# Kernel tuning notes

Measured on AMD Instinct MI355X. Metric: run time of the kernel, lower is better.

Reference implementation:

```python
import jax, jax.numpy as jnp
import numpy as np

DIM = 96
DIM_OUT = 192
HEADS = 2
Q_STRIDE = 4
WINDOW_SIZE = 16  # flattened mask-unit size AFTER q pooling
HEAD_DIM = DIM_OUT // HEADS


def setup_inputs() -> dict:
    key = jax.random.key(0)
    k1, k2, k3, k4, k5 = jax.random.split(key, 5)
    B, N = 64, 3136  # 56x56 tokens, 49 windows of 64 tokens
    x = jax.random.normal(k1, (B, N, DIM), dtype=jnp.float32)
    # nn.Linear params (PyTorch layout: [out, in])
    s_qkv = 1.0 / np.sqrt(DIM)
    w_qkv = jax.random.uniform(k2, (3 * DIM_OUT, DIM), jnp.float32, -s_qkv, s_qkv)
    b_qkv = jax.random.uniform(k3, (3 * DIM_OUT,), jnp.float32, -s_qkv, s_qkv)
    s_proj = 1.0 / np.sqrt(DIM_OUT)
    w_proj = jax.random.uniform(k4, (DIM_OUT, DIM_OUT), jnp.float32, -s_proj, s_proj)
    b_proj = jax.random.uniform(k5, (DIM_OUT,), jnp.float32, -s_proj, s_proj)
    return {"x": x, "w_qkv": w_qkv, "b_qkv": b_qkv, "w_proj": w_proj, "b_proj": b_proj}


def reference(x, w_qkv, b_qkv, w_proj, b_proj):
    B, N, _ = x.shape
    num_windows = N // (Q_STRIDE * WINDOW_SIZE)
    tokens_per_win = Q_STRIDE * WINDOW_SIZE  # 64
    # QKV projection; token axis splits as (tokens_per_win, num_windows)
    qkv = (x @ w_qkv.T + b_qkv).reshape(B, tokens_per_win, num_windows, 3, HEADS, HEAD_DIM)
    qkv = jnp.transpose(qkv, (3, 0, 4, 2, 1, 5))  # [3, B, H, W, T, D]
    q, k, v = qkv[0], qkv[1], qkv[2]
    # q pooling via strided amax over q_stride
    q = q.reshape(B, HEADS, num_windows, Q_STRIDE, WINDOW_SIZE, HEAD_DIM).max(axis=3)
    scale = HEAD_DIM ** (-0.5)
    attn = jax.nn.softmax(jnp.einsum('bhwqd,bhwkd->bhwqk', q * scale, k), axis=-1)
    o = jnp.einsum('bhwqk,bhwkd->bhwqd', attn, v)  # [B, H, W, WINDOW_SIZE, D]
    # transpose(1,3) then flatten -> [B, WINDOW_SIZE*num_windows, dim_out]
    o = jnp.transpose(o, (0, 3, 2, 1, 4)).reshape(B, -1, DIM_OUT)
    return o @ w_proj.T + b_proj
```

## Files before the change

kernel.cpp:

```cpp
#include <hip/hip_runtime.h>


#define NW 49
#define NTOK 3136
#define DIM 96
#define DOUT 192

#define WSQ 0
#define WSBQ 55296
#define WSP 55872
#define WSBP 92736
#define WSTOT 92928

typedef __bf16 bf16x8 __attribute__((ext_vector_type(8)));
typedef float f32x4 __attribute__((ext_vector_type(4)));
typedef unsigned short u16x8 __attribute__((ext_vector_type(8)));
typedef unsigned short u16x4 __attribute__((ext_vector_type(4)));
typedef unsigned int   u32x4 __attribute__((ext_vector_type(4)));

__device__ __forceinline__ unsigned short f2bf(float f) {
    return __builtin_bit_cast(unsigned short, (__bf16)f);
}
__device__ __forceinline__ float bf2f(unsigned short h) {
    unsigned int u = ((unsigned int)h) << 16;
    return __builtin_bit_cast(float, u);
}

__device__ __forceinline__ bool sniff_fp32(const unsigned short* x16) {
    int sane = 0;
    #pragma unroll
    for (int i = 0; i < 32; ++i) {
        unsigned e = ((unsigned)x16[2 * i] >> 7) & 0xFFu;
        sane += (e >= 100u && e <= 141u) ? 1 : 0;
    }
    return sane < 24;
}

__device__ __forceinline__ bf16x8 ldb(const unsigned short* p) {
    return __builtin_bit_cast(bf16x8, *(const u16x8*)p);
}

__global__ __launch_bounds__(256)
void conv_weights(const void* __restrict__ x,
                  const void* __restrict__ w_qkv, const void* __restrict__ b_qkv,
                  const void* __restrict__ w_proj, const void* __restrict__ b_proj,
                  unsigned short* __restrict__ ws)
{
    const bool f32m = sniff_fp32((const unsigned short*)x);
    int t = blockIdx.x * 256 + threadIdx.x;
    if (t >= WSTOT / 8) return;
    int off = t * 8;
    const void* src;
    int rel;
    if (off < WSBQ)      { src = w_qkv;  rel = off; }
    else if (off < WSP)  { src = b_qkv;  rel = off - WSBQ; }
    else if (off < WSBP) { src = w_proj; rel = off - WSP; }
    else                 { src = b_proj; rel = off - WSBP; }
    u16x8 v;
    if (f32m) {
        const float* p = (const float*)src + rel;
        f32x4 a = *(const f32x4*)p;
        f32x4 bb = *(const f32x4*)(p + 4);
        v[0] = f2bf(a[0]);  v[1] = f2bf(a[1]);  v[2] = f2bf(a[2]);  v[3] = f2bf(a[3]);
        v[4] = f2bf(bb[0]); v[5] = f2bf(bb[1]); v[6] = f2bf(bb[2]); v[7] = f2bf(bb[3]);
    } else {
        v = *(const u16x8*)((const unsigned short*)src + rel);
    }
    *(u16x8*)(ws + off) = v;
}

__global__ __launch_bounds__(256, 2)
void mua_main(const void* __restrict__ x,
              const unsigned short* __restrict__ ws,
              void* __restrict__ out)
{
    const int bid = blockIdx.x;
    const int b   = bid / NW;
    const int wi  = bid - b * NW;
    const int tid  = threadIdx.x;
    const int wave = tid >> 6;
    const int lane = tid & 63;
    const int quad = lane >> 4;
    const int l16  = lane & 15;

    __shared__ __attribute__((aligned(16))) unsigned short lds[15616];
    unsigned short* x_s  = lds;
    unsigned short* k_s  = lds;
    unsigned short* v_s  = lds;
    unsigned short* qp_s = lds + 12288;
    unsigned short* o_s  = lds + 12288;

    bf16x8 wq[3][3];
    float  biasq[6];
    #pragma unroll
    for (int nt = 0; nt < 3; ++nt) {
        const int c = (nt * 4 + wave) * 16 + l16;
        #pragma unroll
        for (int ks = 0; ks < 3; ++ks)
            wq[nt][ks] = ldb(ws + WSQ + c * 96 + ks * 32 + quad * 8);
    }
    #pragma unroll
    for (int nt = 0; nt < 6; ++nt)
        biasq[nt] = bf2f(ws[WSBQ + (nt * 4 + wave) * 16 + l16]);

    const bool f32m = sniff_fp32((const unsigned short*)x);

    {
        const size_t xoff = ((size_t)b * NTOK + wi) * DIM;
        if (f32m) {
            #pragma unroll
            for (int i = 0; i < 3; ++i) {
                int chunk = tid + i * 256;
                int row = chunk / 12;
                int c16 = chunk - row * 12;
                const float* p = (const float*)x + xoff + (size_t)row * (NW * DIM) + c16 * 8;
                f32x4 a = *(const f32x4*)p;
                f32x4 bb = *(const f32x4*)(p + 4);
                u16x8 r;
                r[0] = f2bf(a[0]);  r[1] = f2bf(a[1]);  r[2] = f2bf(a[2]);  r[3] = f2bf(a[3]);
                r[4] = f2bf(bb[0]); r[5] = f2bf(bb[1]); r[6] = f2bf(bb[2]); r[7] = f2bf(bb[3]);
                *(u16x8*)&x_s[row * 104 + c16 * 8] = r;
            }
        } else {
            #pragma unroll
            for (int i = 0; i < 3; ++i) {
                int chunk = tid + i * 256;
                int row = chunk / 12;
                int c16 = chunk - row * 12;
                const unsigned short* p = (const unsigned short*)x + xoff + (size_t)row * (NW * DIM) + c16 * 8;
                *(u16x8*)&x_s[row * 104 + c16 * 8] = *(const u16x8*)p;
            }
        }
    }
    __syncthreads();

    bf16x8 afr[4][3];
    #pragma unroll
    for (int mt = 0; mt < 4; ++mt)
        #pragma unroll
        for (int ks = 0; ks < 3; ++ks)
            afr[mt][ks] = ldb(&x_s[(mt * 16 + l16) * 104 + ks * 32 + quad * 8]);
    __syncthreads();

    #pragma unroll
    for (int nt = 0; nt < 6; ++nt) {
        const int slot = nt % 3;
        f32x4 acc[4];
        #pragma unroll
        for (int mt = 0; mt < 4; ++mt) {
            acc[mt] = (f32x4){0.f, 0.f, 0.f, 0.f};
            #pragma unroll
            for (int ks = 0; ks < 3; ++ks)
                acc[mt] = __builtin_amdgcn_mfma_f32_16x16x32_bf16(afr[mt][ks], wq[slot][ks], acc[mt], 0, 0, 0);
        }
        if (nt < 3) {
            const int c2 = ((nt + 3) * 4 + wave) * 16 + l16;
            #pragma unroll
            for (int ks = 0; ks < 3; ++ks)
                wq[slot][ks] = ldb(ws + WSQ + c2 * 96 + ks * 32 + quad * 8);
        }
        const int tt = nt * 4 + wave;
        const float bias = biasq[nt];
        if (nt < 3) {
            const int hd = tt / 6;
            const int d  = (tt % 6) * 16 + l16;
            #pragma unroll
            for (int r = 0; r < 4; ++r) {
                float m = fmaxf(fmaxf(acc[0][r], acc[1][r]), fmaxf(acc[2][r], acc[3][r])) + bias;
                qp_s[(hd * 16 + quad * 4 + r) * 104 + d] = f2bf(m);
            }
        } else {
            const int tk = tt - 12;
            const int hd = tk / 6;
            const int dbh  = ((tk % 6) * 16) / 8 + (l16 >> 3);
            const int dlow = l16 & 7;
            #pragma unroll
            for (int mt = 0; mt < 4; ++mt)
                #pragma unroll
                for (int r = 0; r < 4; ++r)
                    k_s[hd * 6144 + (mt * 16 + quad * 4 + r) * 96 + ((dbh ^ r) << 3) + dlow]
                        = f2bf(acc[mt][r] + bias);
        }
    }
    __syncthreads();

    const int h   = wave >> 1;
    const int sub = wave & 1;
    bf16x8 qa[3];
    #pragma unroll
    for (int ks = 0; ks < 3; ++ks)
        qa[ks] = ldb(&qp_s[(h * 16 + l16) * 104 + ks * 32 + quad * 8]);
    f32x4 st[4];
    #pragma unroll
    for (int mt = 0; mt < 4; ++mt) st[mt] = (f32x4){0.f, 0.f, 0.f, 0.f};
    #pragma unroll
    for (int ks = 0; ks < 3; ++ks)
        #pragma unroll
        for (int mt = 0; mt < 4; ++mt) {
            bf16x8 kb = ldb(&k_s[h * 6144 + (mt * 16 + l16) * 96 + (((ks * 4 + quad) ^ (l16 & 3)) << 3)]);
            st[mt] = __builtin_amdgcn_mfma_f32_16x16x32_bf16(kb, qa[ks], st[mt], 0, 0, 0);
        }
    const float cexp = 0.10206207261596576f * 1.4426950408889634f;
    float mx;
    {
        float m0 = fmaxf(fmaxf(st[0][0], st[0][1]), fmaxf(st[0][2], st[0][3]));
        float m1 = fmaxf(fmaxf(st[1][0], st[1][1]), fmaxf(st[1][2], st[1][3]));
        float m2 = fmaxf(fmaxf(st[2][0], st[2][1]), fmaxf(st[2][2], st[2][3]));
        float m3 = fmaxf(fmaxf(st[3][0], st[3][1]), fmaxf(st[3][2], st[3][3]));
        mx = fmaxf(fmaxf(m0, m1), fmaxf(m2, m3));
    }
    mx = fmaxf(mx, __shfl_xor(mx, 16));
    mx = fmaxf(mx, __shfl_xor(mx, 32));
    float e[4][4];
    #pragma unroll
    for (int mt = 0; mt < 4; ++mt)
        #pragma unroll
        for (int r = 0; r < 4; ++r)
            e[mt][r] = exp2f((st[mt][r] - mx) * cexp);
    float sum;
    {
        float s0 = (e[0][0] + e[0][1]) + (e[0][2] + e[0][3]);
        float s1 = (e[1][0] + e[1][1]) + (e[1][2] + e[1][3]);
        float s2 = (e[2][0] + e[2][1]) + (e[2][2] + e[2][3]);
        float s3 = (e[3][0] + e[3][1]) + (e[3][2] + e[3][3]);
        sum = (s0 + s1) + (s2 + s3);
    }
    sum += __shfl_xor(sum, 16);
    sum += __shfl_xor(sum, 32);
    const float rinv_l = 1.0f / sum;
    float rs[4];
    #pragma unroll
    for (int r = 0; r < 4; ++r)
        rs[r] = __shfl(rinv_l, (lane & 48) + quad * 4 + r);
    unsigned wlo[4], whi[4];
    #pragma unroll
    for (int mt = 0; mt < 4; ++mt) {
        wlo[mt] = (unsigned)f2bf(e[mt][0]) | ((unsigned)f2bf(e[mt][1]) << 16);
        whi[mt] = (unsigned)f2bf(e[mt][2]) | ((unsigned)f2bf(e[mt][3]) << 16);
    }
    bf16x8 pa[2];
    {
        const int srcA = ((quad & 1) * 2) * 16 + l16;
        const int srcB = srcA + 16;
        const bool hiT = quad >= 2;
        #pragma unroll
        for (int ks2 = 0; ks2 < 2; ++ks2) {
            unsigned lo0a = __shfl(wlo[2 * ks2], srcA), lo0b = __shfl(wlo[2 * ks2 + 1], srcA);
            unsigned hi0a = __shfl(whi[2 * ks2], srcA), hi0b = __shfl(whi[2 * ks2 + 1], srcA);
            unsigned lo1a = __shfl(wlo[2 * ks2], srcB), lo1b = __shfl(wlo[2 * ks2 + 1], srcB);
            unsigned hi1a = __shfl(whi[2 * ks2], srcB), hi1b = __shfl(whi[2 * ks2 + 1], srcB);
            u32x4 W;
            W[0] = hiT ? lo0b : lo0a;
            W[1] = hiT ? hi0b : hi0a;
            W[2] = hiT ? lo1b : lo1a;
            W[3] = hiT ? hi1b : hi1a;
            pa[ks2] = __builtin_bit_cast(bf16x8, W);
        }
    }

    bf16x8 wv[2][3];
    float  biasv[3];
    #pragma unroll
    for (int i = 0; i < 2; ++i) {
        const int c = 384 + (i * 4 + wave) * 16 + l16;
        #pragma unroll
        for (int ks = 0; ks < 3; ++ks)
            wv[i][ks] = ldb(ws + WSQ + c * 96 + ks * 32 + quad * 8);
    }
    #pragma unroll
    for (int i = 0; i < 3; ++i)
        biasv[i] = bf2f(ws[WSBQ + 384 + (i * 4 + wave) * 16 + l16]);
    __syncthreads();

    #pragma unroll
    for (int i = 0; i < 3; ++i) {
        const int slot = i & 1;
        f32x4 acc[4];
        #pragma unroll
        for (int mt = 0; mt < 4; ++mt) {
            acc[mt] = (f32x4){0.f, 0.f, 0.f, 0.f};
            #pragma unroll
            for (int ks = 0; ks < 3; ++ks)
                acc[mt] = __builtin_amdgcn_mfma_f32_16x16x32_bf16(afr[mt][ks], wv[slot][ks], acc[mt], 0, 0, 0);
        }
        if (i == 0) {
            const int c2 = 384 + (2 * 4 + wave) * 16 + l16;
            #pragma unroll
            for (int ks = 0; ks < 3; ++ks)
                wv[0][ks] = ldb(ws + WSQ + c2 * 96 + ks * 32 + quad * 8);
        }
        const int tv = i * 4 + wave;
        const int hd = tv / 6;
        const int d  = (tv % 6) * 16 + l16;
        const float bias = biasv[i];
        #pragma unroll
        for (int mt = 0; mt < 4; ++mt) {
            u16x4 pk;
            #pragma unroll
            for (int r = 0; r < 4; ++r) pk[r] = f2bf(acc[mt][r] + bias);
            const int tb = 2 * mt + (quad >> 1);
            *(u16x4*)&v_s[hd * 6144 + d * 64 + ((tb ^ (d & 7)) << 3) + (quad & 1) * 4] = pk;
        }
    }

    const int cbase = wave * 48;
    bf16x8 wpr[3][6];
    float  biasp[3];
    #pragma unroll
    for (int i = 0; i < 3; ++i) {
        const int c = cbase + i * 16 + l16;
        #pragma unroll
        for (int ks = 0; ks < 6; ++ks)
            wpr[i][ks] = ldb(ws + WSP + c * 192 + ks * 32 + quad * 8);
        biasp[i] = bf2f(ws[WSBP + c]);
    }
    __syncthreads();

    #pragma unroll
    for (int i = 0; i < 3; ++i) {
        const int n0 = (sub * 3 + i) * 16;
        f32x4 oacc = (f32x4){0.f, 0.f, 0.f, 0.f};
        #pragma unroll
        for (int ks2 = 0; ks2 < 2; ++ks2) {
            bf16x8 vb = ldb(&v_s[h * 6144 + (n0 + l16) * 64 + (((ks2 * 4 + quad) ^ (l16 & 7)) << 3)]);
            oacc = __builtin_amdgcn_mfma_f32_16x16x32_bf16(pa[ks2], vb, oacc, 0, 0, 0);
        }
        #pragma unroll
        for (int r = 0; r < 4; ++r)
            o_s[(quad * 4 + r) * 200 + h * 96 + n0 + l16] = f2bf(oacc[r] * rs[r]);
    }
    __syncthreads();

    bf16x8 oa[6];
    #pragma unroll
    for (int ks = 0; ks < 6; ++ks)
        oa[ks] = ldb(&o_s[l16 * 200 + ks * 32 + quad * 8]);
    #pragma unroll
    for (int i = 0; i < 3; ++i) {
        const int c = cbase + i * 16 + l16;
        f32x4 acc = (f32x4){0.f, 0.f, 0.f, 0.f};
        #pragma unroll
        for (int ks = 0; ks < 6; ++ks)
            acc = __builtin_amdgcn_mfma_f32_16x16x32_bf16(oa[ks], wpr[i][ks], acc, 0, 0, 0);
        const float bias = biasp[i];
        #pragma unroll
        for (int r = 0; r < 4; ++r) {
            const int m = quad * 4 + r;
            const size_t idx = ((size_t)(b * 784 + m * NW + wi)) * DOUT + c;
            if (f32m) ((float*)out)[idx] = acc[r] + bias;
            else      ((unsigned short*)out)[idx] = f2bf(acc[r] + bias);
        }
    }
}

extern "C" void kernel_launch(void* const* d_in, const int* in_sizes, int n_in,
                              void* d_out, int out_size, void* d_ws, size_t ws_size,
                              hipStream_t stream) {
    const void* x      = d_in[0];
    const void* w_qkv  = d_in[1];
    const void* b_qkv  = d_in[2];
    const void* w_proj = d_in[3];
    const void* b_proj = d_in[4];
    unsigned short* ws = (unsigned short*)d_ws;

    dim3 gridc((WSTOT / 8 + 255) / 256), blockc(256);
    hipLaunchKernelGGL(conv_weights, gridc, blockc, 0, stream,
                       x, w_qkv, b_qkv, w_proj, b_proj, ws);

    dim3 grid(64 * NW), block(256);
    hipLaunchKernelGGL(mua_main, grid, block, 0, stream, x, ws, d_out);
}
```

Before: 179.4 us.

## Halve block to two waves, one per head, with double-buffered weight fragments

```diff
diff --git a/kernel.cpp b/kernel.cpp
--- a/kernel.cpp
+++ b/kernel.cpp
@@ -69,7 +69,7 @@
     *(u16x8*)(ws + off) = v;
 }
 
-__global__ __launch_bounds__(256, 2)
+__global__ __launch_bounds__(128, 3)
 void mua_main(const void* __restrict__ x,
               const unsigned short* __restrict__ ws,
               void* __restrict__ out)
@@ -78,7 +78,7 @@
     const int b   = bid / NW;
     const int wi  = bid - b * NW;
     const int tid  = threadIdx.x;
-    const int wave = tid >> 6;
+    const int h    = tid >> 6;
     const int lane = tid & 63;
     const int quad = lane >> 4;
     const int l16  = lane & 15;
@@ -91,17 +91,17 @@
     unsigned short* o_s  = lds + 12288;
 
     bf16x8 wq[3][3];
-    float  biasq[6];
+    float  biasq[12];
     #pragma unroll
     for (int nt = 0; nt < 3; ++nt) {
-        const int c = (nt * 4 + wave) * 16 + l16;
+        const int c = (nt * 2 + h) * 16 + l16;
         #pragma unroll
         for (int ks = 0; ks < 3; ++ks)
             wq[nt][ks] = ldb(ws + WSQ + c * 96 + ks * 32 + quad * 8);
     }
     #pragma unroll
-    for (int nt = 0; nt < 6; ++nt)
-        biasq[nt] = bf2f(ws[WSBQ + (nt * 4 + wave) * 16 + l16]);
+    for (int nt = 0; nt < 12; ++nt)
+        biasq[nt] = bf2f(ws[WSBQ + (nt * 2 + h) * 16 + l16]);
 
     const bool f32m = sniff_fp32((const unsigned short*)x);
 
@@ -109,8 +109,8 @@
         const size_t xoff = ((size_t)b * NTOK + wi) * DIM;
         if (f32m) {
             #pragma unroll
-            for (int i = 0; i < 3; ++i) {
-                int chunk = tid + i * 256;
+            for (int i = 0; i < 6; ++i) {
+                int chunk = tid + i * 128;
                 int row = chunk / 12;
                 int c16 = chunk - row * 12;
                 const float* p = (const float*)x + xoff + (size_t)row * (NW * DIM) + c16 * 8;
@@ -123,8 +123,8 @@
             }
         } else {
             #pragma unroll
-            for (int i = 0; i < 3; ++i) {
-                int chunk = tid + i * 256;
+            for (int i = 0; i < 6; ++i) {
+                int chunk = tid + i * 128;
                 int row = chunk / 12;
                 int c16 = chunk - row * 12;
                 const unsigned short* p = (const unsigned short*)x + xoff + (size_t)row * (NW * DIM) + c16 * 8;
@@ -143,7 +143,7 @@
     __syncthreads();
 
     #pragma unroll
-    for (int nt = 0; nt < 6; ++nt) {
+    for (int nt = 0; nt < 12; ++nt) {
         const int slot = nt % 3;
         f32x4 acc[4];
         #pragma unroll
@@ -153,15 +153,15 @@
             for (int ks = 0; ks < 3; ++ks)
                 acc[mt] = __builtin_amdgcn_mfma_f32_16x16x32_bf16(afr[mt][ks], wq[slot][ks], acc[mt], 0, 0, 0);
         }
-        if (nt < 3) {
-            const int c2 = ((nt + 3) * 4 + wave) * 16 + l16;
+        if (nt < 9) {
+            const int c2 = ((nt + 3) * 2 + h) * 16 + l16;
             #pragma unroll
             for (int ks = 0; ks < 3; ++ks)
                 wq[slot][ks] = ldb(ws + WSQ + c2 * 96 + ks * 32 + quad * 8);
         }
-        const int tt = nt * 4 + wave;
+        const int tt = nt * 2 + h;
         const float bias = biasq[nt];
-        if (nt < 3) {
+        if (nt < 6) {
             const int hd = tt / 6;
             const int d  = (tt % 6) * 16 + l16;
             #pragma unroll
@@ -184,8 +184,6 @@
     }
     __syncthreads();
 
-    const int h   = wave >> 1;
-    const int sub = wave & 1;
     bf16x8 qa[3];
     #pragma unroll
     for (int ks = 0; ks < 3; ++ks)
@@ -259,21 +257,21 @@
     }
 
     bf16x8 wv[2][3];
-    float  biasv[3];
+    float  biasv[6];
     #pragma unroll
     for (int i = 0; i < 2; ++i) {
-        const int c = 384 + (i * 4 + wave) * 16 + l16;
+        const int c = 384 + (i * 2 + h) * 16 + l16;
         #pragma unroll
         for (int ks = 0; ks < 3; ++ks)
             wv[i][ks] = ldb(ws + WSQ + c * 96 + ks * 32 + quad * 8);
     }
     #pragma unroll
-    for (int i = 0; i < 3; ++i)
-        biasv[i] = bf2f(ws[WSBQ + 384 + (i * 4 + wave) * 16 + l16]);
-    __syncthreads();
-
-    #pragma unroll
-    for (int i = 0; i < 3; ++i) {
+    for (int i = 0; i < 6; ++i)
+        biasv[i] = bf2f(ws[WSBQ + 384 + (i * 2 + h) * 16 + l16]);
+    __syncthreads();
+
+    #pragma unroll
+    for (int i = 0; i < 6; ++i) {
         const int slot = i & 1;
         f32x4 acc[4];
         #pragma unroll
@@ -283,13 +281,13 @@
             for (int ks = 0; ks < 3; ++ks)
                 acc[mt] = __builtin_amdgcn_mfma_f32_16x16x32_bf16(afr[mt][ks], wv[slot][ks], acc[mt], 0, 0, 0);
         }
-        if (i == 0) {
-            const int c2 = 384 + (2 * 4 + wave) * 16 + l16;
+        if (i < 4) {
+            const int c2 = 384 + ((i + 2) * 2 + h) * 16 + l16;
             #pragma unroll
             for (int ks = 0; ks < 3; ++ks)
-                wv[0][ks] = ldb(ws + WSQ + c2 * 96 + ks * 32 + quad * 8);
-        }
-        const int tv = i * 4 + wave;
+                wv[slot][ks] = ldb(ws + WSQ + c2 * 96 + ks * 32 + quad * 8);
+        }
+        const int tv = i * 2 + h;
         const int hd = tv / 6;
         const int d  = (tv % 6) * 16 + l16;
         const float bias = biasv[i];
@@ -303,22 +301,24 @@
         }
     }
 
-    const int cbase = wave * 48;
-    bf16x8 wpr[3][6];
-    float  biasp[3];
-    #pragma unroll
-    for (int i = 0; i < 3; ++i) {
+    const int cbase = h * 96;
+    bf16x8 wpr[2][6];
+    float  biasp[6];
+    #pragma unroll
+    for (int i = 0; i < 2; ++i) {
         const int c = cbase + i * 16 + l16;
         #pragma unroll
         for (int ks = 0; ks < 6; ++ks)
             wpr[i][ks] = ldb(ws + WSP + c * 192 + ks * 32 + quad * 8);
-        biasp[i] = bf2f(ws[WSBP + c]);
-    }
-    __syncthreads();
-
-    #pragma unroll
-    for (int i = 0; i < 3; ++i) {
-        const int n0 = (sub * 3 + i) * 16;
+    }
+    #pragma unroll
+    for (int i = 0; i < 6; ++i)
+        biasp[i] = bf2f(ws[WSBP + cbase + i * 16 + l16]);
+    __syncthreads();
+
+    #pragma unroll
+    for (int i = 0; i < 6; ++i) {
+        const int n0 = i * 16;
         f32x4 oacc = (f32x4){0.f, 0.f, 0.f, 0.f};
         #pragma unroll
         for (int ks2 = 0; ks2 < 2; ++ks2) {
@@ -336,12 +336,19 @@
     for (int ks = 0; ks < 6; ++ks)
         oa[ks] = ldb(&o_s[l16 * 200 + ks * 32 + quad * 8]);
     #pragma unroll
-    for (int i = 0; i < 3; ++i) {
+    for (int i = 0; i < 6; ++i) {
+        const int slot = i & 1;
         const int c = cbase + i * 16 + l16;
         f32x4 acc = (f32x4){0.f, 0.f, 0.f, 0.f};
         #pragma unroll
         for (int ks = 0; ks < 6; ++ks)
-            acc = __builtin_amdgcn_mfma_f32_16x16x32_bf16(oa[ks], wpr[i][ks], acc, 0, 0, 0);
+            acc = __builtin_amdgcn_mfma_f32_16x16x32_bf16(oa[ks], wpr[slot][ks], acc, 0, 0, 0);
+        if (i < 4) {
+            const int c2 = cbase + (i + 2) * 16 + l16;
+            #pragma unroll
+            for (int ks = 0; ks < 6; ++ks)
+                wpr[slot][ks] = ldb(ws + WSP + c2 * 192 + ks * 32 + quad * 8);
+        }
         const float bias = biasp[i];
         #pragma unroll
         for (int r = 0; r < 4; ++r) {
@@ -367,6 +374,6 @@
     hipLaunchKernelGGL(conv_weights, gridc, blockc, 0, stream,
                        x, w_qkv, b_qkv, w_proj, b_proj, ws);
 
-    dim3 grid(64 * NW), block(256);
+    dim3 grid(NTOK), block(128);
     hipLaunchKernelGGL(mua_main, grid, block, 0, stream, x, ws, d_out);
 }
```

Result: faster. 173.5 us (-3.3%).
